# Kernel optimization log

Measured on AMD Instinct MI355X. Metric: run time of the kernel, lower is better.

## Reference

```python
import jax, jax.numpy as jnp
from jax import lax
import numpy as np

NMS_THRESH = 0.5
SCORE_THRESH = 0.05
MAX_DET = 300
B, N, C, P = 8, 20000, 80, 51


def _iou_one_to_many(box, boxes):
    # box: (4,) in (x1,y1,x2,y2); boxes: (N,4). Same IoU math as tf.image.non_max_suppression.
    ix1 = jnp.maximum(box[0], boxes[:, 0])
    iy1 = jnp.maximum(box[1], boxes[:, 1])
    ix2 = jnp.minimum(box[2], boxes[:, 2])
    iy2 = jnp.minimum(box[3], boxes[:, 3])
    inter = jnp.maximum(ix2 - ix1, 0.0) * jnp.maximum(iy2 - iy1, 0.0)
    area_b = (box[2] - box[0]) * (box[3] - box[1])
    area_n = (boxes[:, 2] - boxes[:, 0]) * (boxes[:, 3] - boxes[:, 1])
    union = area_b + area_n - inter
    return jnp.where(union > 0.0, inter / union, 0.0)


def _greedy_nms(boxes, scores):
    """Fixed-length greedy NMS. scores already has -inf at entries below score threshold.
    Returns (idx, keep): idx (MAX_DET,) int32 selected box indices, keep (MAX_DET,) bool validity."""
    bx = lax.stop_gradient(boxes)           # NMS indices are non-differentiable
    s0 = lax.stop_gradient(scores)

    def step(s, _):
        i = jnp.argmax(s)
        ok = s[i] > -jnp.inf
        ious = _iou_one_to_many(bx[i], bx)
        s = jnp.where(ious > NMS_THRESH, -jnp.inf, s)
        s = s.at[i].set(-jnp.inf)
        return s, (i.astype(jnp.int32), ok)

    _, (idx, keep) = lax.scan(step, s0, None, length=MAX_DET)
    return idx, keep


def _filter_one(boxes, classification, relationship):
    # boxes (N,4), classification (N,C), relationship (N,P)
    n_cls = classification.shape[1]
    masked = jnp.where(classification > SCORE_THRESH, classification, -jnp.inf)  # (N,C)
    per_cls = masked.T                                                            # (C,N)

    # class-specific NMS, vectorized over classes
    idx, keep = jax.vmap(lambda s: _greedy_nms(boxes, s))(per_cls)  # (C,MAX_DET) each

    cand = jnp.take_along_axis(per_cls, idx.astype(jnp.int32), axis=1)  # (C,MAX_DET)
    cand = jnp.where(keep, cand, -jnp.inf)

    flat = cand.reshape(-1)                        # (C*MAX_DET,)
    top_s, top_pos = lax.top_k(flat, MAX_DET)      # global top-k over all classes
    box_idx = idx.reshape(-1)[top_pos]             # (MAX_DET,)
    label = top_pos // MAX_DET                     # class id (flatten order (C,M))
    valid = jnp.isfinite(top_s)

    out_boxes = jnp.where(valid[:, None], boxes[box_idx], -1.0)              # (MAX_DET,4)
    out_scores = jnp.where(valid, top_s, -1.0)                               # (MAX_DET,)
    out_labels = jnp.where(valid, label, -1).astype(jnp.int32)

    pred = relationship[box_idx]                                             # (MAX_DET,P)
    pred_labels = jnp.where(valid, jnp.argmax(pred, axis=1), -1).astype(jnp.int32)
    pred_scores = jnp.where(valid, jnp.max(pred, axis=1), -1.0)
    return out_boxes, out_scores, out_labels, pred_scores, pred_labels


def setup_inputs() -> dict:
    key = jax.random.key(0)
    k1, k2, k3, k4 = jax.random.split(key, 4)
    xy = jax.random.uniform(k1, (B, N, 2), dtype=jnp.float32) * 700.0
    wh = jax.random.uniform(k2, (B, N, 2), dtype=jnp.float32) * 100.0 + 1.0
    boxes = jnp.concatenate([xy, xy + wh], axis=-1)                   # valid (x1,y1,x2,y2)
    classification = jax.random.uniform(k3, (B, N, C), dtype=jnp.float32)
    relationship = jax.random.uniform(k4, (B, N, P), dtype=jnp.float32)
    return {"boxes": boxes, "classification": classification, "relationship": relationship}


def reference(boxes, classification, relationship):
    return jax.vmap(_filter_one)(boxes, classification, relationship)
```

## Files before the change

### kernel.cpp

```cpp
#include <hip/hip_runtime.h>
#include <hip/hip_bf16.h>
#include <math.h>

#define NBATCH 8
#define NBOX   20000
#define NCLS   80
#define NREL   51
#define MAXDET 300
#define CAP    512
#define SPECCAP 2560
#define NHB    3328
#define HB0    (0x3F666666u >> 9)
#define TARGETK 480u
#define SCORE_THR 0.05f
#define SPEC_THRF 0.9f
#define WWAVES 8

typedef unsigned long long u64;
typedef unsigned int u32;

__device__ __forceinline__ bool iou_sup(float ax1, float ay1, float ax2, float ay2, float aarea,
                                        float bx1, float by1, float bx2, float by2, float barea) {
  float ix1 = fmaxf(ax1, bx1);
  float iy1 = fmaxf(ay1, by1);
  float ix2 = fminf(ax2, bx2);
  float iy2 = fminf(ay2, by2);
  float dw = fmaxf(__fsub_rn(ix2, ix1), 0.0f);
  float dh = fmaxf(__fsub_rn(iy2, iy1), 0.0f);
  float inter = __fmul_rn(dw, dh);
  float uni = __fsub_rn(__fadd_rn(aarea, barea), inter);
  if (!(uni > 0.0f)) return false;
  return __fdiv_rn(inter, uni) > 0.5f;
}

__device__ __forceinline__ bool iou_gt_half(float ax1, float ay1, float ax2, float ay2,
                                            float bx1, float by1, float bx2, float by2) {
  float aa = __fmul_rn(__fsub_rn(ax2, ax1), __fsub_rn(ay2, ay1));
  float ab = __fmul_rn(__fsub_rn(bx2, bx1), __fsub_rn(by2, by1));
  return iou_sup(ax1, ay1, ax2, ay2, aa, bx1, by1, bx2, by2, ab);
}

__device__ __forceinline__ bool iou_sup_fast(float ax1, float ay1, float ax2, float ay2,
                                             float aarea, float bx1, float by1, float bx2,
                                             float by2, float barea) {
  float ix1 = fmaxf(ax1, bx1);
  float iy1 = fmaxf(ay1, by1);
  float ix2 = fminf(ax2, bx2);
  float iy2 = fminf(ay2, by2);
  float dw = fmaxf(__fsub_rn(ix2, ix1), 0.0f);
  float dh = fmaxf(__fsub_rn(iy2, iy1), 0.0f);
  float inter = __fmul_rn(dw, dh);
  float uni = __fsub_rn(__fadd_rn(aarea, barea), inter);
  return (uni > 0.0f) &&
         ((double)inter * 2.0 > (double)uni * 1.0000000298023223876953125);
}

#define CEXR(x, y, asc) { bool sw_ = (asc) ? ((x) > (y)) : ((x) < (y)); \
                          if (sw_) { u64 t_ = (x); (x) = (y); (y) = t_; } }

__device__ __forceinline__ void bitonic_sort(u64* keys, int SZ, int tid) {
  for (int k = 2; k <= SZ; k <<= 1) {
    for (int j = k >> 1; j >= 4; j >>= 1) {
      for (int v = tid; v < (SZ >> 1); v += 256) {
        int i = ((v & ~(j - 1)) << 1) | (v & (j - 1));
        int p = i | j;
        bool asc = ((i & k) == 0);
        u64 a = keys[i], b = keys[p];
        bool sw = asc ? (a > b) : (a < b);
        if (sw) { keys[i] = b; keys[p] = a; }
      }
      __syncthreads();
    }
    if (tid < (SZ >> 2)) {
      ulonglong2* k2 = (ulonglong2*)keys;
      ulonglong2 lo = k2[tid * 2], hi = k2[tid * 2 + 1];
      u64 a = lo.x, b = lo.y, c = hi.x, d = hi.y;
      int i0 = tid << 2;
      if (k == 2) {
        CEXR(a, b, true); CEXR(c, d, false);
      } else {
        bool asc = ((i0 & k) == 0);
        CEXR(a, c, asc); CEXR(b, d, asc);
        CEXR(a, b, asc); CEXR(c, d, asc);
      }
      lo.x = a; lo.y = b; hi.x = c; hi.y = d;
      k2[tid * 2] = lo; k2[tid * 2 + 1] = hi;
    }
    __syncthreads();
  }
}

template <int NB>
__device__ __forceinline__ void suffix_fast(const u32* hist, u32 cap, u32* wsum4, u32* sout) {
  const int tid = threadIdx.x, lane = tid & 63, w = tid >> 6;
  const int G = NB / 256;
  u32 v = 0;
  const int hb = tid * G;
#pragma unroll
  for (int t = 0; t < G; ++t) v += hist[hb + t];
  u32 s = v;
#pragma unroll
  for (int off = 1; off < 64; off <<= 1) {
    u32 t2 = __shfl_down(s, off);
    if (lane + off < 64) s += t2;
  }
  if (lane == 0) wsum4[w] = s;
  __syncthreads();
  u32 total = wsum4[0] + wsum4[1] + wsum4[2] + wsum4[3];
  u32 after = 0;
#pragma unroll
  for (int ww = 1; ww < 4; ++ww) if (ww > w) after += wsum4[ww];
  u32 inc = s + after;
  u32 exc = inc - v;
  if (tid == 0) sout[3] = total;
  u32 target = total < cap ? total : cap;
  if (total != 0u && inc >= target && exc < target) {
    u32 acc = exc;
    for (int u = hb + G - 1; u >= hb; --u) {
      acc += hist[u];
      if (acc >= target) { sout[0] = (u32)u; sout[1] = acc; sout[2] = acc - hist[u]; break; }
    }
  }
  __syncthreads();
}

__global__ __launch_bounds__(256) void k_tr(const float* __restrict__ cls,
                                            float* __restrict__ colS) {
  __shared__ float tile[NCLS * 65];
  const int tid = threadIdx.x;
  const int b = blockIdx.y;
  const int n0 = blockIdx.x * 64;
  const int rows = (NBOX - n0) < 64 ? (NBOX - n0) : 64;
  const float4* src4 = (const float4*)(cls + ((size_t)b * NBOX + n0) * NCLS);
  const int nq = rows * (NCLS / 4);
  for (int i = tid; i < nq; i += 256) {
    int rr = i / (NCLS / 4);
    int c4 = i - rr * (NCLS / 4);
    float4 v = src4[i];
    tile[(c4 * 4 + 0) * 65 + rr] = v.x;
    tile[(c4 * 4 + 1) * 65 + rr] = v.y;
    tile[(c4 * 4 + 2) * 65 + rr] = v.z;
    tile[(c4 * 4 + 3) * 65 + rr] = v.w;
  }
  __syncthreads();
  float4* dst4 = (float4*)colS;
  for (int i = tid; i < NCLS * 16; i += 256) {
    int c = i >> 4, nl = i & 15;
    if (nl * 4 < rows) {
      float4 v;
      v.x = tile[c * 65 + nl * 4 + 0];
      v.y = tile[c * 65 + nl * 4 + 1];
      v.z = tile[c * 65 + nl * 4 + 2];
      v.w = tile[c * 65 + nl * 4 + 3];
      dst4[(((size_t)b * NCLS + c) * NBOX + n0) / 4 + nl] = v;
    }
  }
}

template <int STRIDE>
__device__ __forceinline__ float4 load4s(const float* col, int q) {
  if (STRIDE == 1) return ((const float4*)col)[q];
  float4 v;
  v.x = col[(size_t)(q * 4 + 0) * STRIDE];
  v.y = col[(size_t)(q * 4 + 1) * STRIDE];
  v.z = col[(size_t)(q * 4 + 2) * STRIDE];
  v.w = col[(size_t)(q * 4 + 3) * STRIDE];
  return v;
}

template <int STRIDE>
__global__ __launch_bounds__(256) void k_sel(const float* __restrict__ scores,
                                             u64* __restrict__ keysBase, size_t kstride,
                                             int* __restrict__ selCnt,
                                             int* __restrict__ totCnt,
                                             int* __restrict__ flags) {
  __shared__ __align__(16) char smem[SPECCAP * 8 + NHB * 4 + CAP * 8];
  u64* side = (u64*)smem;
  u32* hist = (u32*)(smem + SPECCAP * 8);
  u64* keys = (u64*)(smem + SPECCAP * 8 + NHB * 4);
  __shared__ u32 wsum[4], selB[4], twave[4];
  __shared__ u32 s_scnt, s_cnt;

  const int tid = threadIdx.x;
  const int lane = tid & 63;
  const int w = tid >> 6;
  const u64 lmask = (1ull << lane) - 1ull;
  const int bc = blockIdx.x;
  const int b = bc / NCLS, c = bc % NCLS;
  const float* col = (STRIDE == 1) ? (scores + (size_t)bc * NBOX)
                                   : (scores + (size_t)b * NBOX * NCLS + c);

  for (int i = tid; i < NHB; i += 256) hist[i] = 0u;
  if (tid == 0) { s_scnt = 0u; s_cnt = 0u; }
  __syncthreads();

  u32 tailc = 0;
  for (int base = 0; base < NBOX / 4; base += 2048) {
    float4 v[8];
#pragma unroll
    for (int p = 0; p < 8; ++p) {
      int q = base + tid + (p << 8);
      if (q < NBOX / 4) v[p] = load4s<STRIDE>(col, q);
    }
#pragma unroll
    for (int p = 0; p < 8; ++p) {
      int q = base + tid + (p << 8);
      if (q < NBOX / 4) {
        float vv[4] = {v[p].x, v[p].y, v[p].z, v[p].w};
#pragma unroll
        for (int e = 0; e < 4; ++e) {
          float s = vv[e];
          bool spec = s > SPEC_THRF;
          if (s > SCORE_THR && !spec) ++tailc;
          u64 mb = __ballot(spec);
          if (mb) {
            u32 bs;
            if (lane == 0) bs = atomicAdd(&s_scnt, (u32)__popcll(mb));
            bs = __shfl(bs, 0);
            if (spec) {
              u32 bits = __float_as_uint(s);
              u32 pos = bs + (u32)__popcll(mb & lmask);
              if (pos < SPECCAP) side[pos] = ((u64)bits << 32) | (~(u32)(q * 4 + e));
              u32 h = (bits >> 9) - HB0;
              if (h > NHB - 1) h = NHB - 1;
              atomicAdd(&hist[h], 1u);
            }
          }
        }
      }
    }
  }
  u32 tr = tailc;
#pragma unroll
  for (int off = 1; off < 64; off <<= 1) tr += __shfl_down(tr, off);
  if (lane == 0) twave[w] = tr;
  __syncthreads();

  const u32 specCount = s_scnt;
  const u32 tailSum = twave[0] + twave[1] + twave[2] + twave[3];
  const u32 totalAll = specCount + tailSum;

  if (totalAll == 0u) {
    if (tid == 0) { selCnt[bc] = 0; totCnt[bc] = 0; flags[bc] = 0; }
    return;
  }
  const u32 target = totalAll < TARGETK ? totalAll : TARGETK;
  if (specCount < target || specCount > SPECCAP) {
    if (tid == 0) { selCnt[bc] = 0; totCnt[bc] = (int)totalAll; flags[bc] = 1; }
    return;
  }

  suffix_fast<NHB>(hist, target, wsum, selB);
  const u32 F0 = selB[0];
  const u32 selCount = selB[1];
  if (selCount > CAP) {
    if (tid == 0) { selCnt[bc] = 0; totCnt[bc] = (int)totalAll; flags[bc] = 1; }
    return;
  }

  const int iters = (int)((specCount + 255u) >> 8);
  for (int it2 = 0; it2 < iters; ++it2) {
    u32 idx = (u32)it2 * 256u + (u32)tid;
    bool act = idx < specCount;
    u64 key = act ? side[idx] : 0ull;
    u32 bits = (u32)(key >> 32);
    u32 h = (bits >> 9) - HB0;
    if (h > NHB - 1) h = NHB - 1;
    bool sel = act && (h >= F0);
    u64 ms = __ballot(sel);
    if (ms) {
      u32 bs;
      if (lane == 0) bs = atomicAdd(&s_cnt, (u32)__popcll(ms));
      bs = __shfl(bs, 0);
      if (sel) keys[bs + (u32)__popcll(ms & lmask)] = key;
    }
  }
  __syncthreads();
  for (int i = (int)selCount + tid; i < CAP; i += 256) keys[i] = 0ull;
  __syncthreads();

  bitonic_sort(keys, CAP, tid);

  u64* kout = keysBase + (size_t)bc * kstride;
  for (int i = tid; i < CAP; i += 256) kout[i] = keys[i];
  if (tid == 0) { selCnt[bc] = (int)selCount; totCnt[bc] = (int)totalAll; flags[bc] = 0; }
}

__global__ __launch_bounds__(512) void k_walk(const float* __restrict__ boxes,
                                              const u64* __restrict__ keysBase, size_t kstride,
                                              const int* __restrict__ selCnt,
                                              const int* __restrict__ totCnt,
                                              float* __restrict__ keptScore,
                                              int* __restrict__ keptN,
                                              int* __restrict__ keptCount,
                                              int* __restrict__ flags) {
  __shared__ u64 keys[CAP];
  __shared__ float4 candbox[CAP];
  __shared__ float carea[CAP];
  __shared__ float4 keptbox[MAXDET];
  __shared__ float karea[MAXDET];
  __shared__ int kn[MAXDET];
  __shared__ float ksc[MAXDET];
  __shared__ u64 supW[WWAVES];
  __shared__ u64 mpart[WWAVES][64];
  __shared__ int s_kept;

  const int tid = threadIdx.x;
  const int lane = tid & 63;
  const int w = tid >> 6;
  const u64 lmask = (1ull << lane) - 1ull;
  const int bc = blockIdx.x;
  const int b = bc / NCLS;

  if (flags[bc] != 0) return;
  const u32 selCount = (u32)selCnt[bc];
  const u32 totalAll = (u32)totCnt[bc];

  const u64* kin = keysBase + (size_t)bc * kstride;
  for (int i = tid; i < CAP; i += 512) keys[i] = kin[i];
  if (tid == 0) s_kept = 0;
  __syncthreads();

  for (int i = tid; i < (int)selCount; i += 512) {
    int pos = CAP - 1 - i;
    u32 n = ~((u32)keys[pos]);
    float4 bb = ((const float4*)boxes)[(size_t)b * NBOX + n];
    candbox[pos] = bb;
    carea[pos] = __fmul_rn(__fsub_rn(bb.z, bb.x), __fsub_rn(bb.w, bb.y));
  }
  __syncthreads();

  const u32 ntile = (selCount + 63u) >> 6;
  for (u32 t = 0; t < ntile; ++t) {
    const int kept0 = s_kept;
    if (kept0 >= MAXDET) break;
    const u32 r = t * 64u + (u32)lane;
    const bool valid = r < selCount;
    const int si = valid ? (CAP - 1 - (int)r) : (CAP - 1);
    float4 mybox = candbox[si];
    float marea = carea[si];
    bool sup = false;
    for (int k = w; k < kept0; k += WWAVES) {
      float4 kb = keptbox[k];
      if (iou_sup_fast(kb.x, kb.y, kb.z, kb.w, karea[k],
                       mybox.x, mybox.y, mybox.z, mybox.w, marea))
        sup = true;
    }
    u64 bal = __ballot(sup);
    if (lane == 0) supW[w] = bal;
    u64 mw = 0ull;
    const int ebase = w * 8;
#pragma unroll
    for (int ee = 0; ee < 8; ++ee) {
      const int e = ebase + ee;
      int ei = CAP - 1 - (int)(t * 64u) - e;
      float4 eb = candbox[ei];
      if (e < lane && iou_sup_fast(eb.x, eb.y, eb.z, eb.w, carea[ei],
                                   mybox.x, mybox.y, mybox.z, mybox.w, marea))
        mw |= 1ull << e;
    }
    mpart[w][lane] = mw;
    __syncthreads();
    if (w == 0) {
      u64 prior = 0ull, m = 0ull;
#pragma unroll
      for (int ww = 0; ww < WWAVES; ++ww) {
        prior |= supW[ww];
        m |= mpart[ww][lane];
      }
      u64 remaining = __ballot(valid) & ~prior;
      u64 keptmask = 0ull;
      const int room = MAXDET - kept0;
      while (remaining != 0ull && (int)__popcll(keptmask) < room) {
        int j = __ffsll((long long)remaining) - 1;
        keptmask |= 1ull << j;
        remaining &= ~(1ull << j);
        u64 supj = __ballot(((m >> j) & 1ull) != 0ull);
        remaining &= ~supj;
      }
      if ((keptmask >> lane) & 1ull) {
        int pos = kept0 + (int)__popcll(keptmask & lmask);
        u64 mykey = keys[CAP - 1 - (int)r];
        keptbox[pos] = mybox;
        karea[pos] = marea;
        kn[pos] = (int)(~((u32)mykey));
        ksc[pos] = __uint_as_float((u32)(mykey >> 32));
      }
      if (lane == 0) s_kept = kept0 + (int)__popcll(keptmask);
    }
    __syncthreads();
  }

  const int kept = s_kept;
  for (int rr = tid; rr < MAXDET; rr += 512) {
    keptScore[bc * MAXDET + rr] = (rr < kept) ? ksc[rr] : -INFINITY;
    keptN[bc * MAXDET + rr] = (rr < kept) ? kn[rr] : 0;
  }
  if (tid == 0) {
    keptCount[bc] = kept;
    flags[bc] = (kept < MAXDET && selCount < totalAll) ? 1 : 0;
  }
}

__global__ __launch_bounds__(256) void k_slow(const float* __restrict__ boxes,
                                              const float* __restrict__ cls,
                                              float* __restrict__ keptScore,
                                              int* __restrict__ keptN,
                                              int* __restrict__ keptCount,
                                              const int* __restrict__ flags) {
  const int bc = blockIdx.x;
  if (flags[bc] != 1) return;
  const int tid = threadIdx.x;
  const int b = bc / NCLS, c = bc % NCLS;
  const float* col = cls + (size_t)b * NBOX * NCLS + c;
  __shared__ u32 sup[(NBOX + 31) / 32];
  __shared__ u64 red[256];
  __shared__ float4 sbx;
  __shared__ int s_kept;
  for (int i = tid; i < (NBOX + 31) / 32; i += 256) sup[i] = 0u;
  if (tid == 0) s_kept = 0;
  __syncthreads();
  for (int it = 0; it < MAXDET; ++it) {
    u64 best = 0ull;
    for (int n = tid; n < NBOX; n += 256) {
      if ((sup[n >> 5] >> (n & 31)) & 1u) continue;
      float s = col[(size_t)n * NCLS];
      if (s > SCORE_THR) {
        u64 key = ((u64)__float_as_uint(s) << 32) | (~(u32)n);
        if (key > best) best = key;
      }
    }
    red[tid] = best;
    __syncthreads();
    for (int off = 128; off > 0; off >>= 1) {
      if (tid < off) { u64 o = red[tid + off]; if (o > red[tid]) red[tid] = o; }
      __syncthreads();
    }
    u64 win = red[0];
    if (win == 0ull) break;
    u32 nw = ~((u32)win);
    if (tid == 0) {
      int k = s_kept;
      keptScore[bc * MAXDET + k] = __uint_as_float((u32)(win >> 32));
      keptN[bc * MAXDET + k] = (int)nw;
      s_kept = k + 1;
      sbx = ((const float4*)boxes)[(size_t)b * NBOX + nw];
    }
    __syncthreads();
    float4 bx = sbx;
    for (int n = tid; n < NBOX; n += 256) {
      float4 cb = ((const float4*)boxes)[(size_t)b * NBOX + n];
      if (iou_gt_half(bx.x, bx.y, bx.z, bx.w, cb.x, cb.y, cb.z, cb.w))
        atomicOr(&sup[n >> 5], 1u << (n & 31));
    }
    if (tid == 0) atomicOr(&sup[nw >> 5], 1u << (nw & 31));
    __syncthreads();
  }
  __syncthreads();
  const int kept = s_kept;
  for (int r = kept + tid; r < MAXDET; r += 256) {
    keptScore[bc * MAXDET + r] = -INFINITY;
    keptN[bc * MAXDET + r] = 0;
  }
  if (tid == 0) keptCount[bc] = kept;
}

__global__ __launch_bounds__(256) void k_out(const float* __restrict__ boxes,
                                             const float* __restrict__ rel,
                                             const float* __restrict__ keptScore,
                                             const int* __restrict__ keptN,
                                             float* __restrict__ out) {
  __shared__ __align__(16) char smem[NHB * 4 + 1024 * 8];
  u32* hist = (u32*)smem;
  u64* keys = (u64*)(smem + NHB * 4);
  __shared__ u32 wsum[4], selB[4], twave[4];
  __shared__ u32 s_cnt, s_sz;
  const int tid = threadIdx.x;
  const int lane = tid & 63;
  const int w = tid >> 6;
  const u64 lmask = (1ull << lane) - 1ull;
  const int b = blockIdx.x;
  const int NTOT = NCLS * MAXDET;
  const float* ks = keptScore + (size_t)b * NTOT;
  const float4* ks4 = (const float4*)ks;

  for (int i = tid; i < NHB; i += 256) hist[i] = 0u;
  if (tid == 0) s_cnt = 0u;
  __syncthreads();

  u32 tailc = 0;
  for (int base = 0; base < NTOT / 4; base += 2048) {
    float4 v[8];
#pragma unroll
    for (int p = 0; p < 8; ++p) {
      int q = base + tid + (p << 8);
      if (q < NTOT / 4) v[p] = ks4[q];
    }
#pragma unroll
    for (int p = 0; p < 8; ++p) {
      int q = base + tid + (p << 8);
      if (q < NTOT / 4) {
        float vv[4] = {v[p].x, v[p].y, v[p].z, v[p].w};
#pragma unroll
        for (int e = 0; e < 4; ++e) {
          float s = vv[e];
          if (s > SPEC_THRF) {
            u32 h = (__float_as_uint(s) >> 9) - HB0;
            if (h > NHB - 1) h = NHB - 1;
            atomicAdd(&hist[h], 1u);
          } else if (s > 0.0f) {
            ++tailc;
          }
        }
      }
    }
  }
  u32 tr = tailc;
#pragma unroll
  for (int off = 1; off < 64; off <<= 1) tr += __shfl_down(tr, off);
  if (lane == 0) twave[w] = tr;
  __syncthreads();
  const u32 tailSum = twave[0] + twave[1] + twave[2] + twave[3];

  suffix_fast<NHB>(hist, (u32)MAXDET, wsum, selB);
  const u32 specCount = selB[3];
  const u32 totalAll = specCount + tailSum;
  const u32 target = totalAll < (u32)MAXDET ? totalAll : (u32)MAXDET;
  const u32 F0 = selB[0];
  const u32 selSpec = selB[1];

  bool fast = (totalAll != 0u) && (specCount >= target) && (selSpec <= (u32)CAP);

  if (totalAll != 0u) {
    if (fast) {
      for (int base = 0; base < NTOT / 4; base += 2048) {
        float4 v[8];
#pragma unroll
        for (int p = 0; p < 8; ++p) {
          int q = base + tid + (p << 8);
          if (q < NTOT / 4) v[p] = ks4[q];
        }
#pragma unroll
        for (int p = 0; p < 8; ++p) {
          int q = base + tid + (p << 8);
          if (q < NTOT / 4) {
            float vv[4] = {v[p].x, v[p].y, v[p].z, v[p].w};
#pragma unroll
            for (int e = 0; e < 4; ++e) {
              float s = vv[e];
              bool sel = false;
              u32 bits = 0;
              if (s > SPEC_THRF) {
                bits = __float_as_uint(s);
                u32 h = (bits >> 9) - HB0;
                if (h > NHB - 1) h = NHB - 1;
                sel = (h >= F0);
              }
              u64 ms = __ballot(sel);
              if (ms) {
                u32 bs;
                if (lane == 0) bs = atomicAdd(&s_cnt, (u32)__popcll(ms));
                bs = __shfl(bs, 0);
                if (sel)
                  keys[bs + (u32)__popcll(ms & lmask)] =
                      ((u64)bits << 32) | (~(u32)(q * 4 + e));
              }
            }
          }
        }
      }
      if (tid == 0) s_sz = (u32)CAP;
      __syncthreads();
      for (int i = (int)selSpec + tid; i < CAP; i += 256) keys[i] = 0ull;
      __syncthreads();
      bitonic_sort(keys, CAP, tid);
    } else {
      if (tid == 0) s_sz = 1024u;
      __syncthreads();
      if (tid < 64) {
        const int c0 = lane, c1 = 64 + lane;
        const bool has1 = (c1 < NCLS);
        const float* ls0 = keptScore + ((size_t)b * NCLS + c0) * MAXDET;
        const float* ls1 = keptScore + ((size_t)b * NCLS + (has1 ? c1 : c0)) * MAXDET;
        int h0 = 0, h1 = 0;
        float v0 = ls0[0], w0v = ls0[1];
        float v1 = has1 ? ls1[0] : -INFINITY;
        float w1v = has1 ? ls1[1] : -INFINITY;
        for (int r = 0; r < (int)target; ++r) {
          float bs; int bcl;
          if (has1 && v1 > v0) { bs = v1; bcl = c1; } else { bs = v0; bcl = c0; }
#pragma unroll
          for (int off = 32; off > 0; off >>= 1) {
            float os = __shfl_xor(bs, off);
            int oc = __shfl_xor(bcl, off);
            if (os > bs || (os == bs && oc < bcl)) { bs = os; bcl = oc; }
          }
          if (bcl == c0) {
            keys[1023 - r] = ((u64)__float_as_uint(bs) << 32) | (~(u32)(c0 * MAXDET + h0));
            ++h0; v0 = w0v; w0v = (h0 + 1 < MAXDET) ? ls0[h0 + 1] : -INFINITY;
          } else if (has1 && bcl == c1) {
            keys[1023 - r] = ((u64)__float_as_uint(bs) << 32) | (~(u32)(c1 * MAXDET + h1));
            ++h1; v1 = w1v; w1v = (h1 + 1 < MAXDET) ? ls1[h1 + 1] : -INFINITY;
          }
        }
      }
      __syncthreads();
    }
  }

  const int SZr = (totalAll != 0u) ? (int)s_sz : 0;
  for (int r = tid; r < MAXDET; r += 256) {
    const bool valid = (u32)r < target;
    float s = -1.0f, pm = -1.0f, pl = -1.0f, cl = -1.0f;
    float4 ob; ob.x = ob.y = ob.z = ob.w = -1.0f;
    if (valid) {
      u64 key = keys[SZr - 1 - r];
      u32 fp = ~((u32)key);
      int c = (int)(fp / MAXDET);
      int slot = (int)(fp - (u32)c * MAXDET);
      int n = keptN[((size_t)b * NCLS + c) * MAXDET + slot];
      s = __uint_as_float((u32)(key >> 32));
      cl = (float)c;
      size_t nb = (size_t)b * NBOX + (u32)n;
      ob = ((const float4*)boxes)[nb];
      const float* rp = rel + nb * NREL;
      float best = rp[0]; int bi = 0;
      for (int p = 1; p < NREL; ++p) { float vv = rp[p]; if (vv > best) { best = vv; bi = p; } }
      pm = best; pl = (float)bi;
    }
    ((float4*)out)[(size_t)b * MAXDET + r] = ob;
    const int sbase = NBATCH * MAXDET * 4;
    out[sbase + b * MAXDET + r] = s;
    out[sbase + NBATCH * MAXDET + b * MAXDET + r] = cl;
    out[sbase + 2 * NBATCH * MAXDET + b * MAXDET + r] = pm;
    out[sbase + 3 * NBATCH * MAXDET + b * MAXDET + r] = pl;
  }
}

extern "C" void kernel_launch(void* const* d_in, const int* in_sizes, int n_in,
                              void* d_out, int out_size, void* d_ws, size_t ws_size,
                              hipStream_t stream) {
  (void)in_sizes; (void)n_in; (void)out_size;
  const float* boxes = (const float*)d_in[0];
  const float* cls   = (const float*)d_in[1];
  const float* rel   = (const float*)d_in[2];
  float* out = (float*)d_out;
  char* ws = (char*)d_ws;

  const size_t trBytes = (size_t)NBATCH * NCLS * NBOX * 4;
  const size_t NP = NBATCH * NCLS;
  const size_t keptBytes = NP * MAXDET * 8 + NP * 16;
  const bool useTr = ws_size >= trBytes + keptBytes + (size_t)NP * CAP * 8;

  float* colS = (float*)ws;
  char* kbase = useTr ? (ws + trBytes) : ws;
  float* keptScore = (float*)kbase;
  int* keptN = (int*)(kbase + NP * MAXDET * 4);
  int* keptCount = (int*)(kbase + NP * MAXDET * 8);
  int* flags = keptCount + NP;
  int* selCnt = flags + NP;
  int* totCnt = selCnt + NP;
  u64* keysSep = (u64*)(kbase + NP * MAXDET * 8 + NP * 16);

  u64* keysBase = useTr ? (u64*)colS : keysSep;
  const size_t kstride = useTr ? (size_t)(NBOX / 2) : (size_t)CAP;

  if (useTr) {
    k_tr<<<dim3((NBOX + 63) / 64, NBATCH), 256, 0, stream>>>(cls, colS);
    k_sel<1><<<NP, 256, 0, stream>>>(colS, keysBase, kstride, selCnt, totCnt, flags);
  } else {
    k_sel<NCLS><<<NP, 256, 0, stream>>>(cls, keysBase, kstride, selCnt, totCnt, flags);
  }
  k_walk<<<NP, 512, 0, stream>>>(boxes, keysBase, kstride, selCnt, totCnt,
                                 keptScore, keptN, keptCount, flags);
  k_slow<<<NP, 256, 0, stream>>>(boxes, cls, keptScore, keptN, keptCount, flags);
  k_out<<<NBATCH, 256, 0, stream>>>(boxes, rel, keptScore, keptN, out);
}
```

Baseline: 153.4 us.

## Split final top-k stage into sliced histogram, compaction, and sort kernels

The single per-batch output kernel (8 blocks) is replaced by three kernels. A histogram pass and a key-compaction pass each run over 8 slices per batch and merge through global atomics. A final sort/gather kernel then handles each batch. The aim is to spread the scan of 24000 kept scores across more CUs instead of 8 blocks, at the cost of two extra launches, global atomics, and zeroing the global histogram inside k_tr.

```diff
diff --git a/kernel.cpp b/kernel.cpp
--- a/kernel.cpp
+++ b/kernel.cpp
@@ -7,6 +7,7 @@
 #define NCLS   80
 #define NREL   51
 #define MAXDET 300
+#define NTOT   (NCLS * MAXDET)
 #define CAP    512
 #define SPECCAP 2560
 #define NHB    3328
@@ -15,6 +16,8 @@
 #define SCORE_THR 0.05f
 #define SPEC_THRF 0.9f
 #define WWAVES 8
+#define NSLICE 8
+#define QSLICE (NTOT / 4 / NSLICE)
 
 typedef unsigned long long u64;
 typedef unsigned int u32;
@@ -112,7 +115,10 @@
   for (int ww = 1; ww < 4; ++ww) if (ww > w) after += wsum4[ww];
   u32 inc = s + after;
   u32 exc = inc - v;
-  if (tid == 0) sout[3] = total;
+  if (tid == 0) {
+    sout[3] = total;
+    if (total == 0u) { sout[0] = 0u; sout[1] = 0u; sout[2] = 0u; }
+  }
   u32 target = total < cap ? total : cap;
   if (total != 0u && inc >= target && exc < target) {
     u32 acc = exc;
@@ -125,11 +131,22 @@
 }
 
 __global__ __launch_bounds__(256) void k_tr(const float* __restrict__ cls,
-                                            float* __restrict__ colS) {
+                                            float* __restrict__ colS,
+                                            u32* __restrict__ ghist,
+                                            u32* __restrict__ gmisc) {
   __shared__ float tile[NCLS * 65];
   const int tid = threadIdx.x;
   const int b = blockIdx.y;
   const int n0 = blockIdx.x * 64;
+  if (blockIdx.x == 0) {
+    for (int i = tid; i < NHB; i += 256) ghist[b * NHB + i] = 0u;
+    if (tid == 0) {
+      gmisc[b] = 0u;
+      gmisc[NBATCH + b] = 0u;
+      gmisc[2 * NBATCH + b] = 0u;
+      gmisc[3 * NBATCH + b] = 0u;
+    }
+  }
   const int rows = (NBOX - n0) < 64 ? (NBOX - n0) : 64;
   const float4* src4 = (const float4*)(cls + ((size_t)b * NBOX + n0) * NCLS);
   const int nq = rows * (NCLS / 4);
@@ -154,6 +171,19 @@
       v.w = tile[c * 65 + nl * 4 + 3];
       dst4[(((size_t)b * NCLS + c) * NBOX + n0) / 4 + nl] = v;
     }
+  }
+}
+
+__global__ __launch_bounds__(256) void k_zero(u32* __restrict__ ghist,
+                                              u32* __restrict__ gmisc) {
+  const int b = blockIdx.x;
+  const int tid = threadIdx.x;
+  for (int i = tid; i < NHB; i += 256) ghist[b * NHB + i] = 0u;
+  if (tid == 0) {
+    gmisc[b] = 0u;
+    gmisc[NBATCH + b] = 0u;
+    gmisc[2 * NBATCH + b] = 0u;
+    gmisc[3 * NBATCH + b] = 0u;
   }
 }
 
@@ -465,156 +495,165 @@
   if (tid == 0) keptCount[bc] = kept;
 }
 
-__global__ __launch_bounds__(256) void k_out(const float* __restrict__ boxes,
-                                             const float* __restrict__ rel,
-                                             const float* __restrict__ keptScore,
-                                             const int* __restrict__ keptN,
-                                             float* __restrict__ out) {
-  __shared__ __align__(16) char smem[NHB * 4 + 1024 * 8];
-  u32* hist = (u32*)smem;
-  u64* keys = (u64*)(smem + NHB * 4);
-  __shared__ u32 wsum[4], selB[4], twave[4];
-  __shared__ u32 s_cnt, s_sz;
+__global__ __launch_bounds__(256) void k_ohist(const float* __restrict__ keptScore,
+                                               u32* __restrict__ ghist,
+                                               u32* __restrict__ gmisc) {
+  __shared__ u32 hist[NHB];
+  __shared__ u32 twave[4];
   const int tid = threadIdx.x;
   const int lane = tid & 63;
   const int w = tid >> 6;
+  const int b = blockIdx.y;
+  const int sl = blockIdx.x;
+  const float4* ks4 = (const float4*)(keptScore + (size_t)b * NTOT);
+
+  for (int i = tid; i < NHB; i += 256) hist[i] = 0u;
+  __syncthreads();
+
+  u32 tailc = 0;
+  for (int q = sl * QSLICE + tid; q < (sl + 1) * QSLICE; q += 256) {
+    float4 v = ks4[q];
+    float vv[4] = {v.x, v.y, v.z, v.w};
+#pragma unroll
+    for (int e = 0; e < 4; ++e) {
+      float s = vv[e];
+      if (s > SPEC_THRF) {
+        u32 h = (__float_as_uint(s) >> 9) - HB0;
+        if (h > NHB - 1) h = NHB - 1;
+        atomicAdd(&hist[h], 1u);
+      } else if (s > 0.0f) {
+        ++tailc;
+      }
+    }
+  }
+  u32 tr = tailc;
+#pragma unroll
+  for (int off = 1; off < 64; off <<= 1) tr += __shfl_down(tr, off);
+  if (lane == 0 && tr) atomicAdd(&gmisc[b], tr);
+  __syncthreads();
+  for (int i = tid; i < NHB; i += 256) {
+    u32 v = hist[i];
+    if (v) atomicAdd(&ghist[b * NHB + i], v);
+  }
+}
+
+__global__ __launch_bounds__(256) void k_ocomp(const float* __restrict__ keptScore,
+                                               const u32* __restrict__ ghist,
+                                               u32* __restrict__ gmisc,
+                                               u64* __restrict__ keyPool) {
+  __shared__ u32 wsum[4], selB[4];
+  const int tid = threadIdx.x;
+  const int lane = tid & 63;
   const u64 lmask = (1ull << lane) - 1ull;
-  const int b = blockIdx.x;
-  const int NTOT = NCLS * MAXDET;
-  const float* ks = keptScore + (size_t)b * NTOT;
-  const float4* ks4 = (const float4*)ks;
-
-  for (int i = tid; i < NHB; i += 256) hist[i] = 0u;
-  if (tid == 0) s_cnt = 0u;
-  __syncthreads();
-
-  u32 tailc = 0;
-  for (int base = 0; base < NTOT / 4; base += 2048) {
-    float4 v[8];
-#pragma unroll
-    for (int p = 0; p < 8; ++p) {
-      int q = base + tid + (p << 8);
-      if (q < NTOT / 4) v[p] = ks4[q];
-    }
-#pragma unroll
-    for (int p = 0; p < 8; ++p) {
-      int q = base + tid + (p << 8);
-      if (q < NTOT / 4) {
-        float vv[4] = {v[p].x, v[p].y, v[p].z, v[p].w};
-#pragma unroll
-        for (int e = 0; e < 4; ++e) {
-          float s = vv[e];
-          if (s > SPEC_THRF) {
-            u32 h = (__float_as_uint(s) >> 9) - HB0;
-            if (h > NHB - 1) h = NHB - 1;
-            atomicAdd(&hist[h], 1u);
-          } else if (s > 0.0f) {
-            ++tailc;
-          }
-        }
-      }
-    }
-  }
-  u32 tr = tailc;
-#pragma unroll
-  for (int off = 1; off < 64; off <<= 1) tr += __shfl_down(tr, off);
-  if (lane == 0) twave[w] = tr;
-  __syncthreads();
-  const u32 tailSum = twave[0] + twave[1] + twave[2] + twave[3];
-
-  suffix_fast<NHB>(hist, (u32)MAXDET, wsum, selB);
-  const u32 specCount = selB[3];
-  const u32 totalAll = specCount + tailSum;
+  const int b = blockIdx.y;
+  const int sl = blockIdx.x;
+  const float4* ks4 = (const float4*)(keptScore + (size_t)b * NTOT);
+
+  suffix_fast<NHB>(ghist + (size_t)b * NHB, (u32)MAXDET, wsum, selB);
+  const u32 specTotal = selB[3];
+  const u32 tailSum = gmisc[b];
+  const u32 totalAll = specTotal + tailSum;
   const u32 target = totalAll < (u32)MAXDET ? totalAll : (u32)MAXDET;
   const u32 F0 = selB[0];
   const u32 selSpec = selB[1];
-
-  bool fast = (totalAll != 0u) && (specCount >= target) && (selSpec <= (u32)CAP);
-
-  if (totalAll != 0u) {
-    if (fast) {
-      for (int base = 0; base < NTOT / 4; base += 2048) {
-        float4 v[8];
-#pragma unroll
-        for (int p = 0; p < 8; ++p) {
-          int q = base + tid + (p << 8);
-          if (q < NTOT / 4) v[p] = ks4[q];
+  const bool fast = (totalAll != 0u) && (specTotal >= target) && (selSpec <= (u32)CAP);
+
+  if (sl == 0 && tid == 0) {
+    gmisc[3 * NBATCH + b] = target;
+    if (totalAll != 0u && !fast) gmisc[2 * NBATCH + b] = 1u;
+  }
+  if (!fast || totalAll == 0u) return;
+
+  u64* pool = keyPool + (size_t)b * CAP;
+  for (int q = sl * QSLICE + tid; q < (sl + 1) * QSLICE; q += 256) {
+    float4 v = ks4[q];
+    float vv[4] = {v.x, v.y, v.z, v.w};
+#pragma unroll
+    for (int e = 0; e < 4; ++e) {
+      float s = vv[e];
+      bool sel = false;
+      u32 bits = 0;
+      if (s > SPEC_THRF) {
+        bits = __float_as_uint(s);
+        u32 h = (bits >> 9) - HB0;
+        if (h > NHB - 1) h = NHB - 1;
+        sel = (h >= F0);
+      }
+      u64 ms = __ballot(sel);
+      if (ms) {
+        u32 bs;
+        if (lane == 0) bs = atomicAdd(&gmisc[NBATCH + b], (u32)__popcll(ms));
+        bs = __shfl(bs, 0);
+        if (sel) {
+          u32 pos = bs + (u32)__popcll(ms & lmask);
+          if (pos < (u32)CAP) pool[pos] = ((u64)bits << 32) | (~(u32)(q * 4 + e));
         }
-#pragma unroll
-        for (int p = 0; p < 8; ++p) {
-          int q = base + tid + (p << 8);
-          if (q < NTOT / 4) {
-            float vv[4] = {v[p].x, v[p].y, v[p].z, v[p].w};
-#pragma unroll
-            for (int e = 0; e < 4; ++e) {
-              float s = vv[e];
-              bool sel = false;
-              u32 bits = 0;
-              if (s > SPEC_THRF) {
-                bits = __float_as_uint(s);
-                u32 h = (bits >> 9) - HB0;
-                if (h > NHB - 1) h = NHB - 1;
-                sel = (h >= F0);
-              }
-              u64 ms = __ballot(sel);
-              if (ms) {
-                u32 bs;
-                if (lane == 0) bs = atomicAdd(&s_cnt, (u32)__popcll(ms));
-                bs = __shfl(bs, 0);
-                if (sel)
-                  keys[bs + (u32)__popcll(ms & lmask)] =
-                      ((u64)bits << 32) | (~(u32)(q * 4 + e));
-              }
-            }
-          }
+      }
+    }
+  }
+}
+
+__global__ __launch_bounds__(256) void k_osort(const float* __restrict__ boxes,
+                                               const float* __restrict__ rel,
+                                               const float* __restrict__ keptScore,
+                                               const int* __restrict__ keptN,
+                                               const u64* __restrict__ keyPool,
+                                               const u32* __restrict__ gmisc,
+                                               float* __restrict__ out) {
+  __shared__ u64 keys[1024];
+  const int tid = threadIdx.x;
+  const int lane = tid & 63;
+  const int b = blockIdx.x;
+  const u32 target = gmisc[3 * NBATCH + b];
+  const bool fb = gmisc[2 * NBATCH + b] != 0u;
+  int SZ;
+
+  if (!fb) {
+    u32 cnt = gmisc[NBATCH + b];
+    if (cnt > (u32)CAP) cnt = (u32)CAP;
+    const u64* pool = keyPool + (size_t)b * CAP;
+    for (int i = tid; i < CAP; i += 256) keys[i] = (i < (int)cnt) ? pool[i] : 0ull;
+    __syncthreads();
+    bitonic_sort(keys, CAP, tid);
+    SZ = CAP;
+  } else {
+    if (tid < 64) {
+      const int c0 = lane, c1 = 64 + lane;
+      const bool has1 = (c1 < NCLS);
+      const float* ls0 = keptScore + ((size_t)b * NCLS + c0) * MAXDET;
+      const float* ls1 = keptScore + ((size_t)b * NCLS + (has1 ? c1 : c0)) * MAXDET;
+      int h0 = 0, h1 = 0;
+      float v0 = ls0[0], w0v = ls0[1];
+      float v1 = has1 ? ls1[0] : -INFINITY;
+      float w1v = has1 ? ls1[1] : -INFINITY;
+      for (int r = 0; r < (int)target; ++r) {
+        float bs; int bcl;
+        if (has1 && v1 > v0) { bs = v1; bcl = c1; } else { bs = v0; bcl = c0; }
+#pragma unroll
+        for (int off = 32; off > 0; off >>= 1) {
+          float os = __shfl_xor(bs, off);
+          int oc = __shfl_xor(bcl, off);
+          if (os > bs || (os == bs && oc < bcl)) { bs = os; bcl = oc; }
         }
-      }
-      if (tid == 0) s_sz = (u32)CAP;
-      __syncthreads();
-      for (int i = (int)selSpec + tid; i < CAP; i += 256) keys[i] = 0ull;
-      __syncthreads();
-      bitonic_sort(keys, CAP, tid);
-    } else {
-      if (tid == 0) s_sz = 1024u;
-      __syncthreads();
-      if (tid < 64) {
-        const int c0 = lane, c1 = 64 + lane;
-        const bool has1 = (c1 < NCLS);
-        const float* ls0 = keptScore + ((size_t)b * NCLS + c0) * MAXDET;
-        const float* ls1 = keptScore + ((size_t)b * NCLS + (has1 ? c1 : c0)) * MAXDET;
-        int h0 = 0, h1 = 0;
-        float v0 = ls0[0], w0v = ls0[1];
-        float v1 = has1 ? ls1[0] : -INFINITY;
-        float w1v = has1 ? ls1[1] : -INFINITY;
-        for (int r = 0; r < (int)target; ++r) {
-          float bs; int bcl;
-          if (has1 && v1 > v0) { bs = v1; bcl = c1; } else { bs = v0; bcl = c0; }
-#pragma unroll
-          for (int off = 32; off > 0; off >>= 1) {
-            float os = __shfl_xor(bs, off);
-            int oc = __shfl_xor(bcl, off);
-            if (os > bs || (os == bs && oc < bcl)) { bs = os; bcl = oc; }
-          }
-          if (bcl == c0) {
-            keys[1023 - r] = ((u64)__float_as_uint(bs) << 32) | (~(u32)(c0 * MAXDET + h0));
-            ++h0; v0 = w0v; w0v = (h0 + 1 < MAXDET) ? ls0[h0 + 1] : -INFINITY;
-          } else if (has1 && bcl == c1) {
-            keys[1023 - r] = ((u64)__float_as_uint(bs) << 32) | (~(u32)(c1 * MAXDET + h1));
-            ++h1; v1 = w1v; w1v = (h1 + 1 < MAXDET) ? ls1[h1 + 1] : -INFINITY;
-          }
+        if (bcl == c0) {
+          keys[1023 - r] = ((u64)__float_as_uint(bs) << 32) | (~(u32)(c0 * MAXDET + h0));
+          ++h0; v0 = w0v; w0v = (h0 + 1 < MAXDET) ? ls0[h0 + 1] : -INFINITY;
+        } else if (has1 && bcl == c1) {
+          keys[1023 - r] = ((u64)__float_as_uint(bs) << 32) | (~(u32)(c1 * MAXDET + h1));
+          ++h1; v1 = w1v; w1v = (h1 + 1 < MAXDET) ? ls1[h1 + 1] : -INFINITY;
         }
       }
-      __syncthreads();
-    }
-  }
-
-  const int SZr = (totalAll != 0u) ? (int)s_sz : 0;
+    }
+    __syncthreads();
+    SZ = 1024;
+  }
+
   for (int r = tid; r < MAXDET; r += 256) {
     const bool valid = (u32)r < target;
     float s = -1.0f, pm = -1.0f, pl = -1.0f, cl = -1.0f;
     float4 ob; ob.x = ob.y = ob.z = ob.w = -1.0f;
     if (valid) {
-      u64 key = keys[SZr - 1 - r];
+      u64 key = keys[SZ - 1 - r];
       u32 fp = ~((u32)key);
       int c = (int)(fp / MAXDET);
       int slot = (int)(fp - (u32)c * MAXDET);
@@ -649,30 +688,49 @@
 
   const size_t trBytes = (size_t)NBATCH * NCLS * NBOX * 4;
   const size_t NP = NBATCH * NCLS;
-  const size_t keptBytes = NP * MAXDET * 8 + NP * 16;
-  const bool useTr = ws_size >= trBytes + keptBytes + (size_t)NP * CAP * 8;
 
   float* colS = (float*)ws;
+  size_t off = 0;
+  const size_t oKeptScore = off; off += NP * MAXDET * 4;
+  const size_t oKeptN     = off; off += NP * MAXDET * 4;
+  const size_t oKeptCount = off; off += NP * 4;
+  const size_t oFlags     = off; off += NP * 4;
+  const size_t oSelCnt    = off; off += NP * 4;
+  const size_t oTotCnt    = off; off += NP * 4;
+  const size_t oKeysSep   = off; off += NP * CAP * 8;
+  const size_t oGhist     = off; off += (size_t)NBATCH * NHB * 4;
+  const size_t oGmisc     = off; off += 4 * NBATCH * 4;
+  const size_t oKeyPool   = off; off += (size_t)NBATCH * CAP * 8;
+  const size_t kbaseBytes = off;
+
+  const bool useTr = ws_size >= trBytes + kbaseBytes;
   char* kbase = useTr ? (ws + trBytes) : ws;
-  float* keptScore = (float*)kbase;
-  int* keptN = (int*)(kbase + NP * MAXDET * 4);
-  int* keptCount = (int*)(kbase + NP * MAXDET * 8);
-  int* flags = keptCount + NP;
-  int* selCnt = flags + NP;
-  int* totCnt = selCnt + NP;
-  u64* keysSep = (u64*)(kbase + NP * MAXDET * 8 + NP * 16);
+
+  float* keptScore = (float*)(kbase + oKeptScore);
+  int* keptN = (int*)(kbase + oKeptN);
+  int* keptCount = (int*)(kbase + oKeptCount);
+  int* flags = (int*)(kbase + oFlags);
+  int* selCnt = (int*)(kbase + oSelCnt);
+  int* totCnt = (int*)(kbase + oTotCnt);
+  u64* keysSep = (u64*)(kbase + oKeysSep);
+  u32* ghist = (u32*)(kbase + oGhist);
+  u32* gmisc = (u32*)(kbase + oGmisc);
+  u64* keyPool = (u64*)(kbase + oKeyPool);
 
   u64* keysBase = useTr ? (u64*)colS : keysSep;
   const size_t kstride = useTr ? (size_t)(NBOX / 2) : (size_t)CAP;
 
   if (useTr) {
-    k_tr<<<dim3((NBOX + 63) / 64, NBATCH), 256, 0, stream>>>(cls, colS);
+    k_tr<<<dim3((NBOX + 63) / 64, NBATCH), 256, 0, stream>>>(cls, colS, ghist, gmisc);
     k_sel<1><<<NP, 256, 0, stream>>>(colS, keysBase, kstride, selCnt, totCnt, flags);
   } else {
+    k_zero<<<NBATCH, 256, 0, stream>>>(ghist, gmisc);
     k_sel<NCLS><<<NP, 256, 0, stream>>>(cls, keysBase, kstride, selCnt, totCnt, flags);
   }
   k_walk<<<NP, 512, 0, stream>>>(boxes, keysBase, kstride, selCnt, totCnt,
                                  keptScore, keptN, keptCount, flags);
   k_slow<<<NP, 256, 0, stream>>>(boxes, cls, keptScore, keptN, keptCount, flags);
-  k_out<<<NBATCH, 256, 0, stream>>>(boxes, rel, keptScore, keptN, out);
-}
+  k_ohist<<<dim3(NSLICE, NBATCH), 256, 0, stream>>>(keptScore, ghist, gmisc);
+  k_ocomp<<<dim3(NSLICE, NBATCH), 256, 0, stream>>>(keptScore, ghist, gmisc, keyPool);
+  k_osort<<<NBATCH, 256, 0, stream>>>(boxes, rel, keptScore, keptN, keyPool, gmisc, out);
+}
```

Measured after the change: 166.7 us. 1.09x slower.
